# Kernel tuning notes

Hardware: AMD Instinct MI355X
Metric: run time of the kernel (lower is better)

Reference implementation:

```python
import jax, jax.numpy as jnp
import numpy as np

B, IN, H = 8192, 1024, 1024


def setup_inputs() -> dict:
    key = jax.random.key(0)
    ks = jax.random.split(key, 20)
    std = 1.0 / np.sqrt(H)
    u = lambda k, shape: jax.random.uniform(k, shape, jnp.float32, -std, std)
    inp = {
        "x": jax.random.normal(ks[0], (B, IN), jnp.float32),
        "hx": jax.random.normal(ks[1], (B, H), jnp.float32),
        "cx": jax.random.normal(ks[2], (B, H), jnp.float32),
        "task_id": 0,
        # x2h weights [H, IN] (torch Linear layout) and biases [H]
        "wxi": u(ks[3], (H, IN)), "bxi": u(ks[4], (H,)),
        "wxf": u(ks[5], (H, IN)), "bxf": u(ks[6], (H,)),
        "wxc": u(ks[7], (H, IN)), "bxc": u(ks[8], (H,)),
        "wxo": u(ks[9], (H, IN)), "bxo": u(ks[10], (H,)),
        # h2h weights [H, H] and biases [H]
        "whi": u(ks[11], (H, H)), "bhi": u(ks[12], (H,)),
        "whf": u(ks[13], (H, H)), "bhf": u(ks[14], (H,)),
        "whc": u(ks[15], (H, H)), "bhc": u(ks[16], (H,)),
        "who": u(ks[17], (H, H)), "bho": u(ks[18], (H,)),
    }
    return inp


def reference(x, hx, cx, task_id,
              wxi, bxi, wxf, bxf, wxc, bxc, wxo, bxo,
              whi, bhi, whf, bhf, whc, bhc, who, bho):
    # x = x.view(-1, x.size(1)) is identity for 2D input
    # gate pre-activations: Linear(x) + Linear(hx)  (torch: x @ W.T + b)
    ingate = x @ wxi.T + bxi + hx @ whi.T + bhi
    forgetgate = x @ wxf.T + bxf + hx @ whf.T + bhf
    cellgate = x @ wxc.T + bxc + hx @ whc.T + bhc
    outgate = x @ wxo.T + bxo + hx @ who.T + bho

    i = jax.nn.sigmoid(ingate)
    f = jax.nn.sigmoid(forgetgate)
    g = jnp.tanh(cellgate)
    o = jax.nn.sigmoid(outgate)

    cy = cx * f + i * g
    hy = o * jnp.tanh(cy)
    return hy, cy
```

## Files before the change

### kernel.cpp

```cpp
#include <hip/hip_runtime.h>
#include <hip/hip_bf16.h>

#define B_DIM  8192
#define IN_DIM 1024
#define H_DIM  1024
#define K_DIM  2048
#define NT     (K_DIM / 64)

typedef __attribute__((ext_vector_type(8))) short bf16x8;
typedef __attribute__((ext_vector_type(4))) float f32x4;

__device__ __forceinline__ void mfma_16x16x32_bf16(f32x4& d, const bf16x8& a, const bf16x8& b) {
  asm("v_mfma_f32_16x16x32_bf16 %0, %1, %2, %0" : "+v"(d) : "v"(a), "v"(b));
}

__device__ __forceinline__ void gload16(const void* g, void* l) {
  __builtin_amdgcn_global_load_lds(
      (const __attribute__((address_space(1))) void*)g,
      (__attribute__((address_space(3))) void*)l,
      16, 0, 0);
}

__device__ __forceinline__ float fast_sigmoid(float x) {
  return 1.0f / (1.0f + __expf(-x));
}
__device__ __forceinline__ float fast_tanh(float x) {
  float e = __expf(2.0f * x);
  return 1.0f - 2.0f / (e + 1.0f);
}

__global__ __launch_bounds__(256) void pack_a_kernel(
    const float* __restrict__ x, const float* __restrict__ hx,
    __hip_bfloat16* __restrict__ A) {
  const int idx = blockIdx.x * 256 + threadIdx.x;
  const int r  = idx >> 8;
  const int kk = (idx & 255) << 3;
  const float* src = (kk < IN_DIM) ? (x + (size_t)r * IN_DIM + kk)
                                   : (hx + (size_t)r * H_DIM + (kk - IN_DIM));
  const float4 v0 = ((const float4*)src)[0];
  const float4 v1 = ((const float4*)src)[1];
  __hip_bfloat16 t[8];
  t[0] = __float2bfloat16(v0.x); t[1] = __float2bfloat16(v0.y);
  t[2] = __float2bfloat16(v0.z); t[3] = __float2bfloat16(v0.w);
  t[4] = __float2bfloat16(v1.x); t[5] = __float2bfloat16(v1.y);
  t[6] = __float2bfloat16(v1.z); t[7] = __float2bfloat16(v1.w);
  *(uint4*)(A + ((size_t)idx << 3)) = *(const uint4*)t;
}

__global__ __launch_bounds__(256) void pack_w_kernel(
    const float* __restrict__ wxi, const float* __restrict__ wxf,
    const float* __restrict__ wxc, const float* __restrict__ wxo,
    const float* __restrict__ whi, const float* __restrict__ whf,
    const float* __restrict__ whc, const float* __restrict__ who,
    __hip_bfloat16* __restrict__ W) {
  const int idx = blockIdx.x * 256 + threadIdx.x;
  const int row = idx >> 8;
  const int kk  = (idx & 255) << 3;
  const int g = row >> 10, n = row & 1023;
  const float* src;
  if (kk < IN_DIM) {
    const float* p = (g == 0) ? wxi : (g == 1) ? wxf : (g == 2) ? wxc : wxo;
    src = p + (size_t)n * IN_DIM + kk;
  } else {
    const float* p = (g == 0) ? whi : (g == 1) ? whf : (g == 2) ? whc : who;
    src = p + (size_t)n * H_DIM + (kk - IN_DIM);
  }
  const float4 v0 = ((const float4*)src)[0];
  const float4 v1 = ((const float4*)src)[1];
  __hip_bfloat16 t[8];
  t[0] = __float2bfloat16(v0.x); t[1] = __float2bfloat16(v0.y);
  t[2] = __float2bfloat16(v0.z); t[3] = __float2bfloat16(v0.w);
  t[4] = __float2bfloat16(v1.x); t[5] = __float2bfloat16(v1.y);
  t[6] = __float2bfloat16(v1.z); t[7] = __float2bfloat16(v1.w);
  *(uint4*)(W + ((size_t)idx << 3)) = *(const uint4*)t;
}

struct PhaseRegs {
  f32x4 (&acc)[4][8];
  const bf16x8 (&bfr)[4][2];
};

template<int MB>
__device__ __forceinline__ void do_phase(
    const __hip_bfloat16 (*sAp)[64], f32x4 (&acc)[4][8],
    const bf16x8 (&bfr)[4][2], int arow, int chk0, int chk1) {
  bf16x8 a00 = *(const bf16x8*)&sAp[arow + MB * 16][chk0];
  bf16x8 a01 = *(const bf16x8*)&sAp[arow + MB * 16][chk1];
  bf16x8 a10 = *(const bf16x8*)&sAp[arow + (MB + 1) * 16][chk0];
  bf16x8 a11 = *(const bf16x8*)&sAp[arow + (MB + 1) * 16][chk1];
  __builtin_amdgcn_s_setprio(1);
#pragma unroll
  for (int g = 0; g < 4; ++g) {
    mfma_16x16x32_bf16(acc[g][MB],     a00, bfr[g][0]);
    mfma_16x16x32_bf16(acc[g][MB],     a01, bfr[g][1]);
    mfma_16x16x32_bf16(acc[g][MB + 1], a10, bfr[g][0]);
    mfma_16x16x32_bf16(acc[g][MB + 1], a11, bfr[g][1]);
  }
  __builtin_amdgcn_s_setprio(0);
}

__global__ __launch_bounds__(512, 2) void lstm_gemm_kernel(
    const __hip_bfloat16* __restrict__ A,
    const __hip_bfloat16* __restrict__ W,
    const float* __restrict__ cx,
    const float* __restrict__ bxi, const float* __restrict__ bhi,
    const float* __restrict__ bxf, const float* __restrict__ bhf,
    const float* __restrict__ bxc, const float* __restrict__ bhc,
    const float* __restrict__ bxo, const float* __restrict__ bho,
    float* __restrict__ hy, float* __restrict__ cy) {

  __shared__ __align__(16) __hip_bfloat16 sA[2][256][64];
  __shared__ __align__(16) __hip_bfloat16 sW[2][4][64][64];

  const int tid  = threadIdx.x;
  const int w    = tid >> 6;
  const int lane = tid & 63;
  const int wm = w >> 2, wn = w & 3;
  const int lq = lane >> 4, lr16 = lane & 15;

  const int bid = blockIdx.x;
  const int swz = (bid & 7) * 64 + (bid >> 3);
  const int row0 = (swz >> 4) * 256;
  const int col0 = (swz & 15) * 64;

  const int srow = tid >> 3;
  const int scs  = (tid & 7) ^ (srow & 7);
  const __hip_bfloat16* Asrc = A + (size_t)(row0 + srow) * K_DIM + scs * 8;
  const __hip_bfloat16* Wsrc = W + (size_t)(col0 + srow) * K_DIM + scs * 8;
  const size_t Wg = (size_t)H_DIM * K_DIM;

  const int chk0 = ((lq)     ^ (lr16 & 7)) * 8;
  const int chk1 = ((4 + lq) ^ (lr16 & 7)) * 8;
  const int arow = wm * 128 + lr16;
  const int wrow = wn * 16 + lr16;

  f32x4 acc[4][8];
#pragma unroll
  for (int g = 0; g < 4; ++g)
#pragma unroll
    for (int m = 0; m < 8; ++m)
      acc[g][m] = (f32x4){0.f, 0.f, 0.f, 0.f};

#define ISSUE_W2(P, KT, G0)                                                    \
  {                                                                            \
    const size_t kof = (size_t)(KT) * 64;                                      \
    gload16(Wsrc + (size_t)(G0) * Wg + kof,                                    \
            (char*)&sW[P][G0][0][0] + tid * 16);                               \
    gload16(Wsrc + (size_t)((G0) + 1) * Wg + kof,                              \
            (char*)&sW[P][(G0) + 1][0][0] + tid * 16);                         \
  }
#define ISSUE_A2(P, KT, R0, R1)                                                \
  {                                                                            \
    const size_t kof = (size_t)(KT) * 64;                                      \
    gload16(Asrc + (size_t)(R0) * K_DIM + kof,                                 \
            (char*)&sA[P][R0][0] + tid * 16);                                  \
    gload16(Asrc + (size_t)(R1) * K_DIM + kof,                                 \
            (char*)&sA[P][R1][0] + tid * 16);                                  \
  }

  ISSUE_W2(0, 0, 0);
  ISSUE_W2(0, 0, 2);
  ISSUE_A2(0, 0, 0, 128);
  ISSUE_A2(0, 0, 64, 192);

  for (int t = 0; t < NT; ++t) {
    const int p  = t & 1;
    const int q  = p ^ 1;
    const int tn = (t + 1 < NT) ? t + 1 : NT - 1;
    const __hip_bfloat16(*sAp)[64] = sA[p];

    ISSUE_W2(q, tn, 0);
    asm volatile("s_waitcnt vmcnt(4)\n\ts_barrier" ::: "memory");
    bf16x8 bfr[4][2];
#pragma unroll
    for (int g = 0; g < 4; ++g) {
      bfr[g][0] = *(const bf16x8*)&sW[p][g][wrow][chk0];
      bfr[g][1] = *(const bf16x8*)&sW[p][g][wrow][chk1];
    }
    do_phase<0>(sAp, acc, bfr, arow, chk0, chk1);

    ISSUE_W2(q, tn, 2);
    do_phase<2>(sAp, acc, bfr, arow, chk0, chk1);

    ISSUE_A2(q, tn, 0, 128);
    asm volatile("s_waitcnt vmcnt(6)\n\ts_barrier" ::: "memory");
    do_phase<4>(sAp, acc, bfr, arow, chk0, chk1);

    ISSUE_A2(q, tn, 64, 192);
    do_phase<6>(sAp, acc, bfr, arow, chk0, chk1);
  }

  const int h = col0 + wrow;
  const float bi = bxi[h] + bhi[h];
  const float bf = bxf[h] + bhf[h];
  const float bc = bxc[h] + bhc[h];
  const float bo = bxo[h] + bho[h];
#pragma unroll
  for (int m = 0; m < 8; ++m) {
#pragma unroll
    for (int j = 0; j < 4; ++j) {
      const int r = row0 + wm * 128 + m * 16 + lq * 4 + j;
      const size_t o = (size_t)r * H_DIM + h;
      const float ig = fast_sigmoid(acc[0][m][j] + bi);
      const float fg = fast_sigmoid(acc[1][m][j] + bf);
      const float gg = fast_tanh   (acc[2][m][j] + bc);
      const float og = fast_sigmoid(acc[3][m][j] + bo);
      const float c  = cx[o] * fg + ig * gg;
      cy[o] = c;
      hy[o] = og * fast_tanh(c);
    }
  }
#undef ISSUE_W2
#undef ISSUE_A2
}

extern "C" void kernel_launch(void* const* d_in, const int* in_sizes, int n_in,
                              void* d_out, int out_size, void* d_ws, size_t ws_size,
                              hipStream_t stream) {
  const float* x   = (const float*)d_in[0];
  const float* hx  = (const float*)d_in[1];
  const float* cx  = (const float*)d_in[2];
  const float* wxi = (const float*)d_in[4];  const float* bxi = (const float*)d_in[5];
  const float* wxf = (const float*)d_in[6];  const float* bxf = (const float*)d_in[7];
  const float* wxc = (const float*)d_in[8];  const float* bxc = (const float*)d_in[9];
  const float* wxo = (const float*)d_in[10]; const float* bxo = (const float*)d_in[11];
  const float* whi = (const float*)d_in[12]; const float* bhi = (const float*)d_in[13];
  const float* whf = (const float*)d_in[14]; const float* bhf = (const float*)d_in[15];
  const float* whc = (const float*)d_in[16]; const float* bhc = (const float*)d_in[17];
  const float* who = (const float*)d_in[18]; const float* bho = (const float*)d_in[19];

  __hip_bfloat16* Abf = (__hip_bfloat16*)d_ws;
  __hip_bfloat16* Wbf = (__hip_bfloat16*)((char*)d_ws + (size_t)B_DIM * K_DIM * 2);

  float* hy  = (float*)d_out;
  float* cyo = (float*)d_out + (size_t)B_DIM * H_DIM;

  pack_a_kernel<<<(B_DIM * K_DIM / 8) / 256, 256, 0, stream>>>(x, hx, Abf);
  pack_w_kernel<<<(4 * H_DIM * K_DIM / 8) / 256, 256, 0, stream>>>(
      wxi, wxf, wxc, wxo, whi, whf, whc, who, Wbf);

  lstm_gemm_kernel<<<dim3(512), 512, 0, stream>>>(
      Abf, Wbf, cx, bxi, bhi, bxf, bhf, bxc, bhc, bxo, bho, hy, cyo);
}
```

Before: 176.2 us.

## Restructure GEMM main loop into 2x2 quadrant phases with bulk tile prefetch

Each K-tile's inner loop now runs as four phases, each covering one half of the M rows by one half of the gates. A and B fragments are reloaded from LDS per quadrant, holding only 4 A fragments and 2 B fragments instead of all 8 B fragments at once. Prefetching now issues all four A-tile loads at the start of the iteration and all four W-tile loads after the first phase, rather than interleaving pairs. A workgroup barrier is added after every phase. This is meant to lower register pressure and reshape the overlap of global-to-LDS loads with MFMA work, at the cost of extra B-fragment LDS reads and more barriers per tile.

```diff
diff --git a/kernel.cpp b/kernel.cpp
--- a/kernel.cpp
+++ b/kernel.cpp
@@ -75,27 +75,42 @@
   *(uint4*)(W + ((size_t)idx << 3)) = *(const uint4*)t;
 }
 
-struct PhaseRegs {
-  f32x4 (&acc)[4][8];
-  const bf16x8 (&bfr)[4][2];
-};
-
-template<int MB>
-__device__ __forceinline__ void do_phase(
-    const __hip_bfloat16 (*sAp)[64], f32x4 (&acc)[4][8],
-    const bf16x8 (&bfr)[4][2], int arow, int chk0, int chk1) {
-  bf16x8 a00 = *(const bf16x8*)&sAp[arow + MB * 16][chk0];
-  bf16x8 a01 = *(const bf16x8*)&sAp[arow + MB * 16][chk1];
-  bf16x8 a10 = *(const bf16x8*)&sAp[arow + (MB + 1) * 16][chk0];
-  bf16x8 a11 = *(const bf16x8*)&sAp[arow + (MB + 1) * 16][chk1];
+
+template<int MH>
+__device__ __forceinline__ void load_af(const __hip_bfloat16 (*sAp)[64],
+                                        bf16x8 (&af)[4][2], int arowbase,
+                                        int chk0, int chk1) {
+#pragma unroll
+  for (int m = 0; m < 4; ++m) {
+    const int row = arowbase + (MH * 4 + m) * 16;
+    af[m][0] = *(const bf16x8*)&sAp[row][chk0];
+    af[m][1] = *(const bf16x8*)&sAp[row][chk1];
+  }
+}
+
+template<int GH>
+__device__ __forceinline__ void load_bf(const __hip_bfloat16 (*sWp)[64][64],
+                                        bf16x8 (&bf)[2][2], int wrow,
+                                        int chk0, int chk1) {
+#pragma unroll
+  for (int gi = 0; gi < 2; ++gi) {
+    bf[gi][0] = *(const bf16x8*)&sWp[GH * 2 + gi][wrow][chk0];
+    bf[gi][1] = *(const bf16x8*)&sWp[GH * 2 + gi][wrow][chk1];
+  }
+}
+
+template<int MH, int GH>
+__device__ __forceinline__ void mfma16(f32x4 (&acc)[4][8],
+                                       const bf16x8 (&af)[4][2],
+                                       const bf16x8 (&bf)[2][2]) {
   __builtin_amdgcn_s_setprio(1);
 #pragma unroll
-  for (int g = 0; g < 4; ++g) {
-    mfma_16x16x32_bf16(acc[g][MB],     a00, bfr[g][0]);
-    mfma_16x16x32_bf16(acc[g][MB],     a01, bfr[g][1]);
-    mfma_16x16x32_bf16(acc[g][MB + 1], a10, bfr[g][0]);
-    mfma_16x16x32_bf16(acc[g][MB + 1], a11, bfr[g][1]);
-  }
+  for (int gi = 0; gi < 2; ++gi)
+#pragma unroll
+    for (int m = 0; m < 4; ++m) {
+      mfma_16x16x32_bf16(acc[GH * 2 + gi][MH * 4 + m], af[m][0], bf[gi][0]);
+      mfma_16x16x32_bf16(acc[GH * 2 + gi][MH * 4 + m], af[m][1], bf[gi][1]);
+    }
   __builtin_amdgcn_s_setprio(0);
 }
 
@@ -131,7 +146,7 @@
 
   const int chk0 = ((lq)     ^ (lr16 & 7)) * 8;
   const int chk1 = ((4 + lq) ^ (lr16 & 7)) * 8;
-  const int arow = wm * 128 + lr16;
+  const int arowbase = wm * 128 + lr16;
   const int wrow = wn * 16 + lr16;
 
   f32x4 acc[4][8];
@@ -141,58 +156,59 @@
     for (int m = 0; m < 8; ++m)
       acc[g][m] = (f32x4){0.f, 0.f, 0.f, 0.f};
 
-#define ISSUE_W2(P, KT, G0)                                                    \
+#define ISSUE_A4(P, KT)                                                        \
   {                                                                            \
     const size_t kof = (size_t)(KT) * 64;                                      \
-    gload16(Wsrc + (size_t)(G0) * Wg + kof,                                    \
-            (char*)&sW[P][G0][0][0] + tid * 16);                               \
-    gload16(Wsrc + (size_t)((G0) + 1) * Wg + kof,                              \
-            (char*)&sW[P][(G0) + 1][0][0] + tid * 16);                         \
-  }
-#define ISSUE_A2(P, KT, R0, R1)                                                \
+    gload16(Asrc + (size_t)0 * 64 * K_DIM + kof, (char*)&sA[P][0][0]   + tid * 16); \
+    gload16(Asrc + (size_t)1 * 64 * K_DIM + kof, (char*)&sA[P][64][0]  + tid * 16); \
+    gload16(Asrc + (size_t)2 * 64 * K_DIM + kof, (char*)&sA[P][128][0] + tid * 16); \
+    gload16(Asrc + (size_t)3 * 64 * K_DIM + kof, (char*)&sA[P][192][0] + tid * 16); \
+  }
+#define ISSUE_W4(P, KT)                                                        \
   {                                                                            \
     const size_t kof = (size_t)(KT) * 64;                                      \
-    gload16(Asrc + (size_t)(R0) * K_DIM + kof,                                 \
-            (char*)&sA[P][R0][0] + tid * 16);                                  \
-    gload16(Asrc + (size_t)(R1) * K_DIM + kof,                                 \
-            (char*)&sA[P][R1][0] + tid * 16);                                  \
-  }
-
-  ISSUE_W2(0, 0, 0);
-  ISSUE_W2(0, 0, 2);
-  ISSUE_A2(0, 0, 0, 128);
-  ISSUE_A2(0, 0, 64, 192);
+    gload16(Wsrc + (size_t)0 * Wg + kof, (char*)&sW[P][0][0][0] + tid * 16);   \
+    gload16(Wsrc + (size_t)1 * Wg + kof, (char*)&sW[P][1][0][0] + tid * 16);   \
+    gload16(Wsrc + (size_t)2 * Wg + kof, (char*)&sW[P][2][0][0] + tid * 16);   \
+    gload16(Wsrc + (size_t)3 * Wg + kof, (char*)&sW[P][3][0][0] + tid * 16);   \
+  }
+
+  ISSUE_A4(0, 0);
+  ISSUE_W4(0, 0);
+
+  bf16x8 af[4][2];
+  bf16x8 bf[2][2];
 
   for (int t = 0; t < NT; ++t) {
-    const int p  = t & 1;
-    const int q  = p ^ 1;
+    const int p = t & 1, q = p ^ 1;
     const int tn = (t + 1 < NT) ? t + 1 : NT - 1;
     const __hip_bfloat16(*sAp)[64] = sA[p];
-
-    ISSUE_W2(q, tn, 0);
+    const __hip_bfloat16(*sWp)[64][64] = sW[p];
+
+    ISSUE_A4(q, tn);
     asm volatile("s_waitcnt vmcnt(4)\n\ts_barrier" ::: "memory");
-    bf16x8 bfr[4][2];
-#pragma unroll
-    for (int g = 0; g < 4; ++g) {
-      bfr[g][0] = *(const bf16x8*)&sW[p][g][wrow][chk0];
-      bfr[g][1] = *(const bf16x8*)&sW[p][g][wrow][chk1];
-    }
-    do_phase<0>(sAp, acc, bfr, arow, chk0, chk1);
-
-    ISSUE_W2(q, tn, 2);
-    do_phase<2>(sAp, acc, bfr, arow, chk0, chk1);
-
-    ISSUE_A2(q, tn, 0, 128);
-    asm volatile("s_waitcnt vmcnt(6)\n\ts_barrier" ::: "memory");
-    do_phase<4>(sAp, acc, bfr, arow, chk0, chk1);
-
-    ISSUE_A2(q, tn, 64, 192);
-    do_phase<6>(sAp, acc, bfr, arow, chk0, chk1);
+    load_af<0>(sAp, af, arowbase, chk0, chk1);
+    load_bf<0>(sWp, bf, wrow, chk0, chk1);
+    mfma16<0, 0>(acc, af, bf);
+    __builtin_amdgcn_s_barrier();
+
+    ISSUE_W4(q, tn);
+    load_bf<1>(sWp, bf, wrow, chk0, chk1);
+    mfma16<0, 1>(acc, af, bf);
+    __builtin_amdgcn_s_barrier();
+
+    load_af<1>(sAp, af, arowbase, chk0, chk1);
+    mfma16<1, 1>(acc, af, bf);
+    __builtin_amdgcn_s_barrier();
+
+    load_bf<0>(sWp, bf, wrow, chk0, chk1);
+    mfma16<1, 0>(acc, af, bf);
+    __builtin_amdgcn_s_barrier();
   }
 
   const int h = col0 + wrow;
   const float bi = bxi[h] + bhi[h];
-  const float bf = bxf[h] + bhf[h];
+  const float bff = bxf[h] + bhf[h];
   const float bc = bxc[h] + bhc[h];
   const float bo = bxo[h] + bho[h];
 #pragma unroll
@@ -202,7 +218,7 @@
       const int r = row0 + wm * 128 + m * 16 + lq * 4 + j;
       const size_t o = (size_t)r * H_DIM + h;
       const float ig = fast_sigmoid(acc[0][m][j] + bi);
-      const float fg = fast_sigmoid(acc[1][m][j] + bf);
+      const float fg = fast_sigmoid(acc[1][m][j] + bff);
       const float gg = fast_tanh   (acc[2][m][j] + bc);
       const float og = fast_sigmoid(acc[3][m][j] + bo);
       const float c  = cx[o] * fg + ig * gg;
@@ -210,8 +226,8 @@
       hy[o] = og * fast_tanh(c);
     }
   }
-#undef ISSUE_W2
-#undef ISSUE_A2
+#undef ISSUE_A4
+#undef ISSUE_W4
 }
 
 extern "C" void kernel_launch(void* const* d_in, const int* in_sizes, int n_in,
```

Measured after the change: 183.1 us. 1.04x slower.
